# Performance work log

Hardware: AMD Instinct MI355X
Metric: run time of the kernel (lower is better)

The kernel has to match this reference:

```python
import jax, jax.numpy as jnp
import numpy as np

B, S, V, D, P, H, L = 8, 512, 256, 1024, 128, 8, 4


def setup_inputs() -> dict:
    key = jax.random.key(0)
    ks = jax.random.split(key, 8)
    tokens = jax.random.normal(ks[0], (B, S, V), dtype=jnp.float32)
    # causal additive mask (0 on/below diagonal, -1e9 above)
    att_mask = jnp.where(jnp.tril(jnp.ones((S, S), dtype=bool)), 0.0, -1e9).astype(jnp.float32)
    embed_W = jax.random.normal(ks[1], (V, D), dtype=jnp.float32) * 0.02
    unembed_W = jax.random.normal(ks[2], (D, V), dtype=jnp.float32) * 0.02
    wq = jax.random.normal(ks[3], (L, H, D, P), dtype=jnp.float32) * 0.02
    wk = jax.random.normal(ks[4], (L, H, D, P), dtype=jnp.float32) * 0.02
    wv = jax.random.normal(ks[5], (L, H, D, P), dtype=jnp.float32) * 0.02
    wo = jax.random.normal(ks[6], (L, H, P, D), dtype=jnp.float32) * 0.02
    return {"tokens": tokens, "att_mask": att_mask, "embed_W": embed_W,
            "unembed_W": unembed_W, "wq": wq, "wk": wk, "wv": wv, "wo": wo}


def reference(tokens, att_mask, embed_W, unembed_W, wq, wk, wv, wo):
    scale = jnp.asarray(P, tokens.dtype) ** 0.5
    stream = jnp.einsum('bsv,vd->bsd', tokens, embed_W)  # embed
    streams = [stream]
    atts = []
    for l in range(L):  # loop over layers (structural); heads are batched
        q = jnp.einsum('bsd,hdp->bhsp', stream, wq[l])
        k = jnp.einsum('bsd,hdp->bhsp', stream, wk[l])
        v = jnp.einsum('bsd,hdp->bhsp', stream, wv[l])
        logit = jnp.einsum('bhqp,bhkp->bhqk', q, k) / scale + att_mask
        att = jax.nn.softmax(logit, axis=-1)            # [B,H,S,S]
        comb = jnp.einsum('bhqk,bhkp->bhqp', att, v)
        delta = jnp.einsum('bhsp,hpd->bsd', comb, wo[l])  # sum over heads
        stream = stream + delta
        streams.append(stream)
        atts.append(att)
    logits = jnp.einsum('bsd,dv->bsv', stream, unembed_W)
    return (logits, jnp.stack(atts), jnp.stack(streams))
```

## Files before the change

kernel.cpp:

```cpp
#include <hip/hip_runtime.h>
#include <math.h>

typedef __bf16 bf16x8 __attribute__((ext_vector_type(8)));
typedef float  f32x4  __attribute__((ext_vector_type(4)));
typedef _Float16 f16x4 __attribute__((ext_vector_type(4)));

#define GLOAD16(g, l) __builtin_amdgcn_global_load_lds( \
    (const __attribute__((address_space(1))) void*)(g), \
    (__attribute__((address_space(3))) void*)(l), 16, 0, 0)

__global__ __launch_bounds__(256) void cvt_bf16(const float* __restrict__ in,
                                                __bf16* __restrict__ out)
{
    const int i = (blockIdx.x * 256 + threadIdx.x) * 4;
    float4 f = *(const float4*)(in + i);
    out[i + 0] = (__bf16)f.x; out[i + 1] = (__bf16)f.y;
    out[i + 2] = (__bf16)f.z; out[i + 3] = (__bf16)f.w;
}

__global__ __launch_bounds__(256) void transpose_cvt(
    const float* __restrict__ in, __bf16* __restrict__ out,
    int C, int outLd, long inZ, int zdiv, long outZ1, long outZ2)
{
    __shared__ float t[32][33];
    const int z = blockIdx.z, z1 = z / zdiv, z2 = z % zdiv;
    in  += (long)z * inZ;
    out += z1 * outZ1 + z2 * outZ2;
    const int c0 = blockIdx.x * 32, r0 = blockIdx.y * 32;
    const int tx = threadIdx.x, ty = threadIdx.y;
    #pragma unroll
    for (int i = 0; i < 32; i += 8)
        t[ty + i][tx] = in[(long)(r0 + ty + i) * C + c0 + tx];
    __syncthreads();
    #pragma unroll
    for (int i = 0; i < 32; i += 8)
        out[(long)(c0 + ty + i) * outLd + r0 + tx] = (__bf16)t[tx][ty + i];
}

__global__ __launch_bounds__(256) void mfma_gemm(
    const __bf16* __restrict__ A, const __bf16* __restrict__ Bt,
    int lda, int ldb, int K,
    float* __restrict__ outF, int ldf,
    __bf16* __restrict__ outB, int ldo,
    __bf16* __restrict__ vt,
    const float* __restrict__ resid, int ldr)
{
    __shared__ __bf16 As[128 * 32];
    __shared__ __bf16 Bs[128 * 32];

    const int m0 = blockIdx.y * 128, n0 = blockIdx.x * 128;
    const int t = threadIdx.x, w = t >> 6, ln = t & 63;
    const int r = ln & 15, q = ln >> 4;
    const int wm = (w >> 1) * 64, wn = (w & 1) * 64;

    f32x4 acc[4][4];
    #pragma unroll
    for (int i = 0; i < 4; ++i)
        #pragma unroll
        for (int j = 0; j < 4; ++j)
            acc[i][j] = f32x4{0.f, 0.f, 0.f, 0.f};

    const int srow = ln >> 2, scol = (ln & 3) * 8;

    for (int k0 = 0; k0 < K; k0 += 32) {
        #pragma unroll
        for (int c = 0; c < 2; ++c) {
            const int ch = w + c * 4;
            const __bf16* ga = A  + (long)(m0 + ch * 16 + srow) * lda + k0 + scol;
            GLOAD16(ga, &As[ch * 512]);
            const __bf16* gb = Bt + (long)(n0 + ch * 16 + srow) * ldb + k0 + scol;
            GLOAD16(gb, &Bs[ch * 512]);
        }
        __syncthreads();
        bf16x8 af[4], bv[4];
        #pragma unroll
        for (int i = 0; i < 4; ++i) af[i] = *(const bf16x8*)&As[(wm + i * 16 + r) * 32 + q * 8];
        #pragma unroll
        for (int i = 0; i < 4; ++i) bv[i] = *(const bf16x8*)&Bs[(wn + i * 16 + r) * 32 + q * 8];
        #pragma unroll
        for (int i = 0; i < 4; ++i)
            #pragma unroll
            for (int j = 0; j < 4; ++j)
                acc[i][j] = __builtin_amdgcn_mfma_f32_16x16x32_bf16(af[i], bv[j], acc[i][j], 0, 0, 0);
        __syncthreads();
    }

    #pragma unroll
    for (int i = 0; i < 4; ++i) {
        #pragma unroll
        for (int j = 0; j < 4; ++j) {
            #pragma unroll
            for (int g = 0; g < 4; ++g) {
                const int m = m0 + wm + i * 16 + q * 4 + g;
                const int n = n0 + wn + j * 16 + r;
                float v = acc[i][j][g];
                if (resid) v += resid[(long)m * ldr + n];
                if (outF)  outF[(long)m * ldf + n] = v;
                if (outB) {
                    if (vt && n >= 2048) {
                        const int p = n - 2048, h = p >> 7, pp = p & 127;
                        const int b = m >> 9, s = m & 511;
                        vt[(((long)(b * 8 + h)) * 128 + pp) * 512 + s] = (__bf16)v;
                    } else {
                        outB[(long)m * ldo + n] = (__bf16)v;
                    }
                }
            }
        }
    }
}

__global__ __launch_bounds__(256, 3) void flash2(
    const __bf16* __restrict__ QK, const __bf16* __restrict__ Vt,
    float* __restrict__ atts, __bf16* __restrict__ comb)
{
    const int f = blockIdx.x;
    const int bh = (f & 7) * 8 + ((f >> 3) & 7);
    const int qt = f >> 6;
    const int b = bh >> 3, h = bh & 7;
    const int nkt = (qt >> 1) + 1;
    const float rs = 0.08838834764831845f;

    __shared__ __bf16 KVs[128 * 136];
    __shared__ __bf16 Ps[4 * 16 * 136];

    const int t = threadIdx.x, w = t >> 6, ln = t & 63;
    const int r = ln & 15, q = ln >> 4;

    const long qrow = (long)(b * 512 + qt * 64 + w * 16 + r);
    bf16x8 Qf[4];
    #pragma unroll
    for (int kp = 0; kp < 4; ++kp)
        Qf[kp] = *(const bf16x8*)(QK + qrow * 2048 + h * 128 + kp * 32 + q * 8);

    f16x4 E16[4][8];
    float L[4] = {0.f, 0.f, 0.f, 0.f};

    #pragma unroll
    for (int kt = 0; kt < 4; ++kt) {
        if (kt < nkt) {
            __syncthreads();
            const __bf16* ksrc = QK + ((long)(b * 512 + kt * 128)) * 2048 + 1024 + h * 128;
            #pragma unroll
            for (int c0 = 0; c0 < 8; ++c0) {
                const int c = c0 * 256 + t;
                const int row = c >> 4, col = (c & 15) * 8;
                *(bf16x8*)&KVs[row * 136 + col] = *(const bf16x8*)(ksrc + (long)row * 2048 + col);
            }
            __syncthreads();

            #pragma unroll
            for (int nb = 0; nb < 8; ++nb) {
                f32x4 s = f32x4{0.f, 0.f, 0.f, 0.f};
                #pragma unroll
                for (int kp = 0; kp < 4; ++kp) {
                    bf16x8 bv = *(const bf16x8*)&KVs[(nb * 16 + r) * 136 + kp * 32 + q * 8];
                    s = __builtin_amdgcn_mfma_f32_16x16x32_bf16(Qf[kp], bv, s, 0, 0, 0);
                }
                const int kc = kt * 128 + nb * 16 + r;
                f16x4 e;
                #pragma unroll
                for (int g = 0; g < 4; ++g) {
                    float ev = __expf(s[g] * rs - 3.0f);
                    if (kt == nkt - 1) {
                        const int qr = qt * 64 + w * 16 + q * 4 + g;
                        if (kc > qr) ev = 0.f;
                    }
                    L[g] += ev;
                    e[g] = (_Float16)ev;
                }
                E16[kt][nb] = e;
            }
        }
    }

    float linv[4];
    #pragma unroll
    for (int g = 0; g < 4; ++g) {
        float Lg = L[g];
        #pragma unroll
        for (int s = 1; s < 16; s <<= 1) Lg += __shfl_xor(Lg, s);
        linv[g] = 1.0f / Lg;
    }

    f32x4 O[8];
    #pragma unroll
    for (int pb = 0; pb < 8; ++pb) O[pb] = f32x4{0.f, 0.f, 0.f, 0.f};

    float* abase = atts + (long)bh * 262144 + (long)(qt * 64 + w * 16) * 512;
    __bf16* psw = &Ps[w * 16 * 136];

    #pragma unroll
    for (int kt = 0; kt < 4; ++kt) {
        if (kt < nkt) {
            __syncthreads();
            const __bf16* vsrc = Vt + (long)bh * 65536 + kt * 128;
            #pragma unroll
            for (int c0 = 0; c0 < 8; ++c0) {
                const int c = c0 * 256 + t;
                const int row = c >> 4, col = (c & 15) * 8;
                *(bf16x8*)&KVs[row * 136 + col] = *(const bf16x8*)(vsrc + (long)row * 512 + col);
            }
            __syncthreads();

            #pragma unroll
            for (int nb = 0; nb < 8; ++nb) {
                f16x4 e = E16[kt][nb];
                #pragma unroll
                for (int g = 0; g < 4; ++g) {
                    float p = (float)e[g] * linv[g];
                    abase[(long)(q * 4 + g) * 512 + kt * 128 + nb * 16 + r] = p;
                    psw[(q * 4 + g) * 136 + nb * 16 + r] = (__bf16)p;
                }
            }
            bf16x8 Pf[4];
            #pragma unroll
            for (int kp = 0; kp < 4; ++kp)
                Pf[kp] = *(const bf16x8*)&psw[r * 136 + kp * 32 + q * 8];
            #pragma unroll
            for (int pb = 0; pb < 8; ++pb) {
                #pragma unroll
                for (int kp = 0; kp < 4; ++kp) {
                    bf16x8 bv = *(const bf16x8*)&KVs[(pb * 16 + r) * 136 + kp * 32 + q * 8];
                    O[pb] = __builtin_amdgcn_mfma_f32_16x16x32_bf16(Pf[kp], bv, O[pb], 0, 0, 0);
                }
            }
        }
    }

    {
        float* zbase = atts + (long)bh * 262144 + (long)(qt * 64) * 512;
        float4 z4 = {0.f, 0.f, 0.f, 0.f};
        for (int ktz = nkt; ktz < 4; ++ktz) {
            #pragma unroll
            for (int c0 = 0; c0 < 8; ++c0) {
                const int c = c0 * 256 + t;
                const int row = c >> 5, col = (c & 31) * 4;
                *(float4*)&zbase[(long)row * 512 + ktz * 128 + col] = z4;
            }
        }
    }

    const long crow = (long)(b * 512 + qt * 64 + w * 16);
    #pragma unroll
    for (int pb = 0; pb < 8; ++pb)
        #pragma unroll
        for (int g = 0; g < 4; ++g)
            comb[(crow + q * 4 + g) * 1024 + h * 128 + pb * 16 + r] = (__bf16)O[pb][g];
}

extern "C" void kernel_launch(void* const* d_in, const int* in_sizes, int n_in,
                              void* d_out, int out_size, void* d_ws, size_t ws_size,
                              hipStream_t stream)
{
    const float* tokens = (const float*)d_in[0];
    const float* embedW = (const float*)d_in[2];
    const float* unembW = (const float*)d_in[3];
    const float* wq     = (const float*)d_in[4];
    const float* wk     = (const float*)d_in[5];
    const float* wv     = (const float*)d_in[6];
    const float* wo     = (const float*)d_in[7];

    float* out       = (float*)d_out;
    float* logits_o  = out;
    float* atts_o    = out + 1048576L;
    float* streams_o = atts_o + 67108864L;

    __bf16* embedWt   = (__bf16*)d_ws;
    __bf16* unembWt   = embedWt + 262144;
    __bf16* WtAll     = unembWt + 262144;
    __bf16* WotAll    = WtAll + 12582912;
    __bf16* tokens_bf = WotAll + 4194304;
    __bf16* stream_bf = tokens_bf + 1048576;
    __bf16* QKbuf     = stream_bf + 4194304;
    __bf16* Vt        = QKbuf + 8388608;
    __bf16* comb      = Vt + 4194304;

    const dim3 T(32, 8), G1(256);

    cvt_bf16<<<dim3(1024), G1, 0, stream>>>(tokens, tokens_bf);
    transpose_cvt<<<dim3(32, 8, 1), T, 0, stream>>>(embedW, embedWt, 1024, 256, 0, 1, 0, 0);
    transpose_cvt<<<dim3(8, 32, 1), T, 0, stream>>>(unembW, unembWt, 256, 1024, 0, 1, 0, 0);
    transpose_cvt<<<dim3(4, 32, 32), T, 0, stream>>>(wq, WtAll,           128, 1024, 131072, 8, 3145728, 131072);
    transpose_cvt<<<dim3(4, 32, 32), T, 0, stream>>>(wk, WtAll + 1048576, 128, 1024, 131072, 8, 3145728, 131072);
    transpose_cvt<<<dim3(4, 32, 32), T, 0, stream>>>(wv, WtAll + 2097152, 128, 1024, 131072, 8, 3145728, 131072);
    transpose_cvt<<<dim3(32, 32, 4), T, 0, stream>>>(wo, WotAll, 1024, 1024, 1048576, 1, 1048576, 0);

    mfma_gemm<<<dim3(8, 32), G1, 0, stream>>>(
        tokens_bf, embedWt, 256, 256, 256,
        streams_o, 1024, stream_bf, 1024, nullptr, nullptr, 0);

    for (int l = 0; l < 4; ++l) {
        float* st  = streams_o + (long)l * 4194304;
        float* stn = st + 4194304;
        float* attl = atts_o + (long)l * 16777216;

        mfma_gemm<<<dim3(24, 32), G1, 0, stream>>>(
            stream_bf, WtAll + (long)l * 3145728, 1024, 1024, 1024,
            nullptr, 0, QKbuf, 2048, Vt, nullptr, 0);

        flash2<<<dim3(512), G1, 0, stream>>>(QKbuf, Vt, attl, comb);

        mfma_gemm<<<dim3(8, 32), G1, 0, stream>>>(
            comb, WotAll + (long)l * 1048576, 1024, 1024, 1024,
            stn, 1024, stream_bf, 1024, nullptr, st, 1024);
    }

    mfma_gemm<<<dim3(2, 32), G1, 0, stream>>>(
        stream_bf, unembWt, 1024, 1024, 1024,
        logits_o, 256, nullptr, 0, nullptr, nullptr, 0);
}
```

Measured before the change: 883.5 us.

## Add 256x256-tile pipelined QKV GEMM with swizzled LDS and XCD-aware block mapping

Replaces the 128x128 QKV projection GEMM with a new 512-thread kernel that uses 256x256 tiles, a 4-slot ring of LDS buffers filled by async global-to-LDS loads three slices ahead, an XOR-swizzled LDS layout to avoid bank conflicts, and raised wave priority around the MFMA block. Blocks are mapped so that each XCD works on a contiguous group of tiles. The remaining mfma_gemm calls also get XCD-grouped block remapping. The aim is more data reuse per tile and memory latency overlapped with compute, at the cost of 128KB of dynamic LDS and one block per CU.

New measurement: 900.3 us. About the same (+1.9%).

```diff
diff --git a/kernel.cpp b/kernel.cpp
--- a/kernel.cpp
+++ b/kernel.cpp
@@ -42,13 +42,16 @@
     int lda, int ldb, int K,
     float* __restrict__ outF, int ldf,
     __bf16* __restrict__ outB, int ldo,
-    __bf16* __restrict__ vt,
     const float* __restrict__ resid, int ldr)
 {
     __shared__ __bf16 As[128 * 32];
     __shared__ __bf16 Bs[128 * 32];
 
-    const int m0 = blockIdx.y * 128, n0 = blockIdx.x * 128;
+    int lid = blockIdx.y * gridDim.x + blockIdx.x;
+    const int nwg = gridDim.x * gridDim.y;
+    lid = (lid & 7) * (nwg >> 3) + (lid >> 3);
+    const int m0 = (lid / gridDim.x) * 128, n0 = (lid % gridDim.x) * 128;
+
     const int t = threadIdx.x, w = t >> 6, ln = t & 63;
     const int r = ln & 15, q = ln >> 4;
     const int wm = (w >> 1) * 64, wn = (w & 1) * 64;
@@ -96,14 +99,110 @@
                 float v = acc[i][j][g];
                 if (resid) v += resid[(long)m * ldr + n];
                 if (outF)  outF[(long)m * ldf + n] = v;
-                if (outB) {
-                    if (vt && n >= 2048) {
-                        const int p = n - 2048, h = p >> 7, pp = p & 127;
-                        const int b = m >> 9, s = m & 511;
-                        vt[(((long)(b * 8 + h)) * 128 + pp) * 512 + s] = (__bf16)v;
-                    } else {
-                        outB[(long)m * ldo + n] = (__bf16)v;
-                    }
+                if (outB)  outB[(long)m * ldo + n] = (__bf16)v;
+            }
+        }
+    }
+}
+
+__device__ __forceinline__ void stage_slice(
+    const __bf16* __restrict__ src, int ld, int row0, int k0,
+    __bf16* ring, int w, int ln)
+{
+    #pragma unroll
+    for (int c = 0; c < 2; ++c) {
+        const int L = 2 * w + c;
+        const int row = L * 16 + (ln >> 2);
+        const int lg = (ln & 3) ^ ((row >> 2) & 3);
+        const __bf16* g = src + (long)(row0 + row) * ld + k0 + lg * 8;
+        GLOAD16(g, ring + L * 512);
+    }
+}
+
+__global__ __launch_bounds__(512, 1) void gemm256(
+    const __bf16* __restrict__ A, const __bf16* __restrict__ Bt,
+    int lda, int ldb, int K,
+    __bf16* __restrict__ outB, __bf16* __restrict__ vt)
+{
+    extern __shared__ char smem[];
+    __bf16* As = (__bf16*)smem;
+    __bf16* Bs = (__bf16*)(smem + 65536);
+
+    const int bid = blockIdx.x;
+    const int xcd = bid & 7, idx = bid >> 3;
+    const int mt = (xcd & 3) * 4 + (idx & 3);
+    const int nt = (xcd >> 2) * 6 + (idx >> 2);
+    const int m0 = mt * 256, n0 = nt * 256;
+
+    const int t = threadIdx.x, w = t >> 6, ln = t & 63;
+    const int r = ln & 15, q = ln >> 4;
+    const int wm = w >> 2, wn = w & 3;
+
+    f32x4 acc[8][4];
+    #pragma unroll
+    for (int i = 0; i < 8; ++i)
+        #pragma unroll
+        for (int jf = 0; jf < 4; ++jf)
+            acc[i][jf] = f32x4{0.f, 0.f, 0.f, 0.f};
+
+    const int nk = K >> 5;
+    #pragma unroll
+    for (int j = 0; j < 3; ++j) {
+        stage_slice(A,  lda, m0, j * 32, As + j * 8192, w, ln);
+        stage_slice(Bt, ldb, n0, j * 32, Bs + j * 8192, w, ln);
+    }
+
+#define GSTEP(J, VM) { \
+    asm volatile("s_waitcnt vmcnt(" #VM ")" ::: "memory"); \
+    __builtin_amdgcn_s_barrier(); \
+    __builtin_amdgcn_sched_barrier(0); \
+    const __bf16* as_ = As + ((J) & 3) * 8192; \
+    const __bf16* bs_ = Bs + ((J) & 3) * 8192; \
+    bf16x8 af[8], bv[4]; \
+    _Pragma("unroll") \
+    for (int i = 0; i < 8; ++i) { \
+        const int row = wm * 128 + i * 16 + r; \
+        af[i] = *(const bf16x8*)&as_[row * 32 + ((q ^ ((row >> 2) & 3)) << 3)]; \
+    } \
+    _Pragma("unroll") \
+    for (int jf = 0; jf < 4; ++jf) { \
+        const int row = wn * 64 + jf * 16 + r; \
+        bv[jf] = *(const bf16x8*)&bs_[row * 32 + ((q ^ ((row >> 2) & 3)) << 3)]; \
+    } \
+    if ((J) + 3 < nk) { \
+        stage_slice(A,  lda, m0, ((J) + 3) * 32, As + (((J) + 3) & 3) * 8192, w, ln); \
+        stage_slice(Bt, ldb, n0, ((J) + 3) * 32, Bs + (((J) + 3) & 3) * 8192, w, ln); \
+    } \
+    __builtin_amdgcn_s_setprio(1); \
+    _Pragma("unroll") \
+    for (int i = 0; i < 8; ++i) \
+        _Pragma("unroll") \
+        for (int jf = 0; jf < 4; ++jf) \
+            acc[i][jf] = __builtin_amdgcn_mfma_f32_16x16x32_bf16(af[i], bv[jf], acc[i][jf], 0, 0, 0); \
+    __builtin_amdgcn_s_setprio(0); \
+}
+
+    for (int j = 0; j < nk - 2; ++j) GSTEP(j, 8);
+    GSTEP(nk - 2, 4);
+    GSTEP(nk - 1, 0);
+#undef GSTEP
+
+    const bool isV = (nt >= 8);
+    #pragma unroll
+    for (int i = 0; i < 8; ++i) {
+        #pragma unroll
+        for (int jf = 0; jf < 4; ++jf) {
+            #pragma unroll
+            for (int g = 0; g < 4; ++g) {
+                const int row = m0 + wm * 128 + i * 16 + q * 4 + g;
+                const int col = n0 + wn * 64 + jf * 16 + r;
+                const __bf16 v = (__bf16)acc[i][jf][g];
+                if (isV) {
+                    const int p = col - 2048, h = p >> 7, pp = p & 127;
+                    const int b = row >> 9, s = row & 511;
+                    vt[(((long)(b * 8 + h)) * 128 + pp) * 512 + s] = v;
+                } else {
+                    outB[(long)row * 2048 + col] = v;
                 }
             }
         }
@@ -278,6 +377,9 @@
 
     const dim3 T(32, 8), G1(256);
 
+    hipFuncSetAttribute((const void*)gemm256,
+                        hipFuncAttributeMaxDynamicSharedMemorySize, 131072);
+
     cvt_bf16<<<dim3(1024), G1, 0, stream>>>(tokens, tokens_bf);
     transpose_cvt<<<dim3(32, 8, 1), T, 0, stream>>>(embedW, embedWt, 1024, 256, 0, 1, 0, 0);
     transpose_cvt<<<dim3(8, 32, 1), T, 0, stream>>>(unembW, unembWt, 256, 1024, 0, 1, 0, 0);
@@ -288,25 +390,25 @@
 
     mfma_gemm<<<dim3(8, 32), G1, 0, stream>>>(
         tokens_bf, embedWt, 256, 256, 256,
-        streams_o, 1024, stream_bf, 1024, nullptr, nullptr, 0);
+        streams_o, 1024, stream_bf, 1024, nullptr, 0);
 
     for (int l = 0; l < 4; ++l) {
         float* st  = streams_o + (long)l * 4194304;
         float* stn = st + 4194304;
         float* attl = atts_o + (long)l * 16777216;
 
-        mfma_gemm<<<dim3(24, 32), G1, 0, stream>>>(
+        gemm256<<<dim3(192), dim3(512), 131072, stream>>>(
             stream_bf, WtAll + (long)l * 3145728, 1024, 1024, 1024,
-            nullptr, 0, QKbuf, 2048, Vt, nullptr, 0);
+            QKbuf, Vt);
 
         flash2<<<dim3(512), G1, 0, stream>>>(QKbuf, Vt, attl, comb);
 
         mfma_gemm<<<dim3(8, 32), G1, 0, stream>>>(
             comb, WotAll + (long)l * 1048576, 1024, 1024, 1024,
-            stn, 1024, stream_bf, 1024, nullptr, st, 1024);
+            stn, 1024, stream_bf, 1024, st, 1024);
     }
 
     mfma_gemm<<<dim3(2, 32), G1, 0, stream>>>(
         stream_bf, unembWt, 1024, 1024, 1024,
-        logits_o, 256, nullptr, 0, nullptr, nullptr, 0);
-}
+        logits_o, 256, nullptr, 0, nullptr, 0);
+}
```
